# Optimization experiments

Hardware: AMD Instinct MI355X
Metric: run time of the kernel (lower is better)

Reference implementation:

```python
import jax, jax.numpy as jnp
import numpy as np

TOP_P = 0.9
B, D, H, O, E = 8192, 1024, 2048, 1024, 8


def setup_inputs() -> dict:
    key = jax.random.key(0)
    ks = jax.random.split(key, 6)
    def init(k, shape, fan_in):
        return (jax.random.normal(k, shape, jnp.float32) * (fan_in ** -0.5)).astype(jnp.float32)
    return {
        "x": jax.random.normal(ks[0], (B, D), jnp.float32),
        "gate_w": init(ks[1], (D, E), D),
        "gate_b": jnp.zeros((E,), jnp.float32),
        "w1": init(ks[2], (E, D, H), D),
        "b1": jnp.zeros((E, H), jnp.float32),
        "w2": init(ks[3], (E, H, O), H),
        "b2": jnp.zeros((E, O), jnp.float32),
    }


def reference(x, gate_w, gate_b, w1, b1, w2, b2):
    # gate + softmax
    logits = x @ gate_w + gate_b                      # [B,E]
    probs = jax.nn.softmax(logits, axis=-1)
    # all-expert MLP (batched over experts); torch GELU default is exact (erf)
    h = jax.nn.gelu(jnp.einsum('bd,edh->beh', x, w1) + b1[None], approximate=False)
    all_out = jnp.einsum('beh,eho->beo', h, w2) + b2[None]  # [B,E,O]
    # routing (entropy) loss
    routing_loss = (-jnp.sum(probs * jnp.log(probs + 1e-8), axis=-1)).mean()
    # diversity (gram logdet) loss
    mean_probs = probs.mean(axis=0)[:, None]          # [E,1]
    expert_mean = all_out.mean(axis=0)                # [E,O]
    norm = jnp.linalg.norm(expert_mean, axis=1, keepdims=True) + 1e-6
    V = mean_probs * (expert_mean / norm)             # [E,O]
    gram = V @ V.T + 1e-6 * jnp.eye(E, dtype=V.dtype)
    diversity_loss = -jnp.linalg.slogdet(gram)[1]
    # top-p mask over experts
    order = jnp.argsort(-probs, axis=-1)              # descending
    p_sorted = jnp.take_along_axis(probs, order, axis=-1)
    cum = jnp.cumsum(p_sorted, axis=-1)
    mask = cum <= TOP_P
    mask = mask.at[:, 0].set(True)
    inv = jnp.argsort(order, axis=-1)                 # inverse permutation
    mask_orig = jnp.take_along_axis(mask, inv, axis=-1)
    # normalized masked combine
    mp = probs * mask_orig.astype(probs.dtype)
    wts = mp / (mp.sum(axis=-1, keepdims=True) + 1e-8)
    output = jnp.einsum('be,beo->bo', wts, all_out)
    return output, routing_loss, diversity_loss
```

## Files before the change

### kernel.cpp

```cpp
#include <hip/hip_runtime.h>
#include <cstdint>
#include <cstddef>
#include <cmath>

#define B_ 8192
#define D_ 1024
#define H_ 2048
#define O_ 1024
#define E_ 8

typedef __bf16 bf16;
typedef __bf16 bf16x8 __attribute__((ext_vector_type(8)));
typedef __bf16 bf16x4v __attribute__((ext_vector_type(4)));
typedef float f32x4 __attribute__((ext_vector_type(4)));

typedef __attribute__((address_space(1))) void gvoid;
typedef __attribute__((address_space(3))) void lvoid;

__device__ __forceinline__ void gload16(const void* g, void* l) {
  __builtin_amdgcn_global_load_lds((gvoid*)g, (lvoid*)l, 16u, 0, 0);
}

__device__ __forceinline__ float fast_erff(float x) {
  float ax = __builtin_fabsf(x);
  float t = 1.f / (1.f + 0.3275911f * ax);
  float p = t * (0.254829592f +
            t * (-0.284496736f +
            t * (1.421413741f +
            t * (-1.453152027f +
            t * 1.061405429f))));
  float r = 1.f - p * __expf(-ax * ax);
  return __builtin_copysignf(r, x);
}
__device__ __forceinline__ float gelu_exact(float v) {
  return 0.5f * v * (1.f + fast_erff(v * 0.70710678118654752f));
}

__global__ __launch_bounds__(256) void convert_x_kernel(const float* __restrict__ x,
                                                        bf16* __restrict__ xb) {
  size_t i = (size_t)blockIdx.x * 256 + threadIdx.x;
  float4 v = ((const float4*)x)[i];
  bf16x4v o;
  o[0] = (bf16)v.x; o[1] = (bf16)v.y; o[2] = (bf16)v.z; o[3] = (bf16)v.w;
  ((bf16x4v*)xb)[i] = o;
}

__global__ __launch_bounds__(256) void transpose_w_kernel(const float* __restrict__ w,
                                                          bf16* __restrict__ wt,
                                                          int R, int C) {
  __shared__ float tile[32][33];
  int e = blockIdx.z;
  int c0 = blockIdx.x * 32, r0 = blockIdx.y * 32;
  int tx = threadIdx.x, ty = threadIdx.y;
  const float* we = w + (size_t)e * R * C;
  bf16* wte = wt + (size_t)e * R * C;
#pragma unroll
  for (int k = 0; k < 4; ++k) {
    int r = ty + 8 * k;
    tile[r][tx] = we[(size_t)(r0 + r) * C + c0 + tx];
  }
  __syncthreads();
#pragma unroll
  for (int k = 0; k < 4; ++k) {
    int c = ty + 8 * k;
    wte[(size_t)(c0 + c) * R + r0 + tx] = (bf16)tile[tx][c];
  }
}

__global__ __launch_bounds__(256) void gating_kernel(const float* __restrict__ x,
                                                     const float* __restrict__ gw,
                                                     const float* __restrict__ gb,
                                                     float* __restrict__ probs,
                                                     float* __restrict__ wts,
                                                     float* __restrict__ ent) {
  int w = threadIdx.x >> 6, l = threadIdx.x & 63;
  int b = blockIdx.x * 4 + w;
  const float* xr = x + (size_t)b * D_;
  float acc[E_];
#pragma unroll
  for (int e = 0; e < E_; ++e) acc[e] = 0.f;
  for (int j = 0; j < D_ / 64; ++j) {
    int d = j * 64 + l;
    float xv = xr[d];
    const float* g = gw + (size_t)d * E_;
#pragma unroll
    for (int e = 0; e < E_; ++e) acc[e] += xv * g[e];
  }
#pragma unroll
  for (int off = 32; off; off >>= 1)
#pragma unroll
    for (int e = 0; e < E_; ++e) acc[e] += __shfl_down(acc[e], off);

  if (l == 0) {
    float lg[E_], p[E_];
    float mx = -1e30f;
#pragma unroll
    for (int e = 0; e < E_; ++e) { lg[e] = acc[e] + gb[e]; mx = fmaxf(mx, lg[e]); }
    float s = 0.f;
#pragma unroll
    for (int e = 0; e < E_; ++e) { p[e] = expf(lg[e] - mx); s += p[e]; }
    float inv = 1.f / s;
    float en = 0.f;
#pragma unroll
    for (int e = 0; e < E_; ++e) { p[e] *= inv; en -= p[e] * logf(p[e] + 1e-8f); }
    ent[b] = en;
#pragma unroll
    for (int e = 0; e < E_; ++e) probs[(size_t)b * E_ + e] = p[e];
    int idx[E_]; float ps[E_];
#pragma unroll
    for (int e = 0; e < E_; ++e) { idx[e] = e; ps[e] = p[e]; }
    for (int i = 0; i < E_ - 1; ++i)
      for (int j = 0; j < E_ - 1 - i; ++j)
        if (ps[j] < ps[j + 1]) {
          float tp = ps[j]; ps[j] = ps[j + 1]; ps[j + 1] = tp;
          int ti = idx[j]; idx[j] = idx[j + 1]; idx[j + 1] = ti;
        }
    float cum = 0.f; float mp[E_];
#pragma unroll
    for (int e = 0; e < E_; ++e) mp[e] = 0.f;
    for (int i = 0; i < E_; ++i) {
      cum += ps[i];
      bool m = (cum <= 0.9f) || (i == 0);
      if (m) mp[idx[i]] = ps[i];
    }
    float ssum = 0.f;
#pragma unroll
    for (int e = 0; e < E_; ++e) ssum += mp[e];
    float invs = 1.f / (ssum + 1e-8f);
#pragma unroll
    for (int e = 0; e < E_; ++e) wts[(size_t)b * E_ + e] = mp[e] * invs;
  }
}

__device__ __forceinline__ void gemm_loop_rs(const bf16* __restrict__ A,
                                             const bf16* __restrict__ Bt,
                                             int K, int rowBase, int colBase,
                                             bf16* lA, bf16* lB, f32x4 acc[4][4]) {
  const int tid = threadIdx.x;
  const int w = tid >> 6, l = tid & 63;
  const int wm = w >> 1, wn = w & 1;
  const int fm = l & 15, fc = l >> 4;
  const int lr = l >> 3;
  const int lc = l & 7;
  const bf16* gA = A + (size_t)(rowBase + w * 32 + lr) * K + lc * 8;
  const bf16* gB = Bt + (size_t)(colBase + w * 32 + lr) * K + lc * 8;
  const int wp = lc ^ lr;
  bf16* dA = lA + (w * 32 + lr) * 64 + wp * 8;
  bf16* dB = lB + (w * 32 + lr) * 64 + wp * 8;

  bf16x8 ra[4], rb[4];
  const int nIter = K >> 6;
#pragma unroll
  for (int i = 0; i < 4; ++i) {
    ra[i] = *(const bf16x8*)(gA + (size_t)(i * 8) * K);
    rb[i] = *(const bf16x8*)(gB + (size_t)(i * 8) * K);
  }
  for (int it = 0; it < nIter; ++it) {
    __syncthreads();
#pragma unroll
    for (int i = 0; i < 4; ++i) {
      *(bf16x8*)(dA + i * 512) = ra[i];
      *(bf16x8*)(dB + i * 512) = rb[i];
    }
    if (it + 1 < nIter) {
      const int k0 = (it + 1) << 6;
#pragma unroll
      for (int i = 0; i < 4; ++i) {
        ra[i] = *(const bf16x8*)(gA + (size_t)(i * 8) * K + k0);
        rb[i] = *(const bf16x8*)(gB + (size_t)(i * 8) * K + k0);
      }
    }
    __syncthreads();
#pragma unroll
    for (int kh = 0; kh < 2; ++kh) {
      bf16x8 af[4], bb[4];
#pragma unroll
      for (int mt = 0; mt < 4; ++mt) {
        int r = wm * 64 + mt * 16 + fm;
        int pos = (kh * 4 + fc) ^ (r & 7);
        af[mt] = *(const bf16x8*)(lA + r * 64 + pos * 8);
      }
#pragma unroll
      for (int nt = 0; nt < 4; ++nt) {
        int r = wn * 64 + nt * 16 + fm;
        int pos = (kh * 4 + fc) ^ (r & 7);
        bb[nt] = *(const bf16x8*)(lB + r * 64 + pos * 8);
      }
#pragma unroll
      for (int mt = 0; mt < 4; ++mt)
#pragma unroll
        for (int nt = 0; nt < 4; ++nt)
          acc[mt][nt] = __builtin_amdgcn_mfma_f32_16x16x32_bf16(af[mt], bb[nt], acc[mt][nt], 0, 0, 0);
    }
  }
}

__device__ __forceinline__ void gemm_loop(const bf16* __restrict__ A,
                                          const bf16* __restrict__ Bt,
                                          int K, int rowBase, int colBase,
                                          bf16* lA, bf16* lB, f32x4 acc[4][4]) {
  const int tid = threadIdx.x;
  const int w = tid >> 6, l = tid & 63;
  const int wm = w >> 1, wn = w & 1;
  const int fm = l & 15, fc = l >> 4;
  const int lr = l >> 2, lc = l & 3;
  const int sr0 = (w * 2 + 0) * 16 + lr;
  const int sr1 = (w * 2 + 1) * 16 + lr;
  const int cg0 = lc ^ ((sr0 >> 1) & 3);
  const int cg1 = lc ^ ((sr1 >> 1) & 3);
  const bf16* gA0 = A + (size_t)(rowBase + sr0) * K + cg0 * 8;
  const bf16* gA1 = A + (size_t)(rowBase + sr1) * K + cg1 * 8;
  const bf16* gB0 = Bt + (size_t)(colBase + sr0) * K + cg0 * 8;
  const bf16* gB1 = Bt + (size_t)(colBase + sr1) * K + cg1 * 8;
  bf16* lA0 = lA + (w * 2 + 0) * 512;
  bf16* lA1 = lA + (w * 2 + 1) * 512;
  bf16* lB0 = lB + (w * 2 + 0) * 512;
  bf16* lB1 = lB + (w * 2 + 1) * 512;

  for (int k0 = 0; k0 < K; k0 += 32) {
    __syncthreads();
    gload16(gA0 + k0, lA0);
    gload16(gA1 + k0, lA1);
    gload16(gB0 + k0, lB0);
    gload16(gB1 + k0, lB1);
    __syncthreads();

    bf16x8 af[4], bb[4];
#pragma unroll
    for (int mt = 0; mt < 4; ++mt) {
      int r = wm * 64 + mt * 16 + fm;
      af[mt] = *(const bf16x8*)(lA + (size_t)(r * 4 + (fc ^ ((r >> 1) & 3))) * 8);
    }
#pragma unroll
    for (int nt = 0; nt < 4; ++nt) {
      int r = wn * 64 + nt * 16 + fm;
      bb[nt] = *(const bf16x8*)(lB + (size_t)(r * 4 + (fc ^ ((r >> 1) & 3))) * 8);
    }
#pragma unroll
    for (int mt = 0; mt < 4; ++mt)
#pragma unroll
      for (int nt = 0; nt < 4; ++nt)
        acc[mt][nt] = __builtin_amdgcn_mfma_f32_16x16x32_bf16(af[mt], bb[nt], acc[mt][nt], 0, 0, 0);
  }
}

__global__ __launch_bounds__(256) void gemm1_v5_kernel(const bf16* __restrict__ xb,
                                                       const bf16* __restrict__ w1t,
                                                       const float* __restrict__ b1,
                                                       const float* __restrict__ wts,
                                                       bf16* __restrict__ h_chunk,
                                                       float* __restrict__ hsum,
                                                       int rowOffset, int Bc) {
  __shared__ bf16 smem[17408];
  bf16* lA = smem;
  bf16* lB = smem + 8192;
  f32x4 acc[4][4];
#pragma unroll
  for (int mt = 0; mt < 4; ++mt)
#pragma unroll
    for (int nt = 0; nt < 4; ++nt) acc[mt][nt] = 0.f;

  const int flat = blockIdx.y * 128 + blockIdx.x;
  const int xcd = flat & 7, lin = flat >> 3;
  const int cb = xcd * 16 + (lin & 15);
  const int rb = lin >> 4;
  const int colBase = cb * 128;
  const int rowLocal = rb * 128;
  const int rowGlobal = rowOffset + rowLocal;
  const int e = colBase >> 11;

  gemm_loop_rs(xb, w1t, D_, rowGlobal, colBase, lA, lB, acc);

  const int tid = threadIdx.x;
  const int w = tid >> 6, l = tid & 63;
  const int wm = w >> 1, wn = w & 1;
  const int fm = l & 15, fc = l >> 4;
  bf16* he = h_chunk + (size_t)e * Bc * H_;
  const int hc0 = colBase & (H_ - 1);

  float wgt[4][4];
#pragma unroll
  for (int mt = 0; mt < 4; ++mt)
#pragma unroll
    for (int i = 0; i < 4; ++i) {
      int gr = rowGlobal + wm * 64 + mt * 16 + fc * 4 + i;
      wgt[mt][i] = wts[(size_t)gr * E_ + e];
    }

  __syncthreads();
#pragma unroll
  for (int nt = 0; nt < 4; ++nt) {
    int c = wn * 64 + nt * 16 + fm;
    float bias = b1[colBase + c];
    float csum = 0.f;
#pragma unroll
    for (int mt = 0; mt < 4; ++mt) {
      int rbse = wm * 64 + mt * 16 + fc * 4;
#pragma unroll
      for (int i = 0; i < 4; ++i) {
        float v = gelu_exact(acc[mt][nt][i] + bias);
        csum += v;
        smem[(size_t)(rbse + i) * 136 + c] = (bf16)(v * wgt[mt][i]);
      }
    }
    csum += __shfl_down(csum, 32);
    csum += __shfl_down(csum, 16);
    if (fc == 0) atomicAdd(&hsum[colBase + c], csum);
  }
  __syncthreads();

#pragma unroll
  for (int j = 0; j < 8; ++j) {
    int row = j * 16 + (tid >> 4);
    int cchunk = tid & 15;
    bf16x8 v = *(const bf16x8*)(smem + (size_t)row * 136 + cchunk * 8);
    *(bf16x8*)(he + (size_t)(rowLocal + row) * H_ + hc0 + cchunk * 8) = v;
  }
}

template <int SPLIT>
__global__ __launch_bounds__(256) void gemm2_v5_kernel(const bf16* __restrict__ h_chunk,
                                                       const bf16* __restrict__ w2t,
                                                       const float* __restrict__ b2,
                                                       const float* __restrict__ wts,
                                                       float* __restrict__ out_chunk,
                                                       int rowOffset, int Bc) {
  __shared__ bf16 smem[16384];
  bf16* lA = smem;
  bf16* lB = smem + 8192;
  f32x4 acc[4][4];
#pragma unroll
  for (int mt = 0; mt < 4; ++mt)
#pragma unroll
    for (int nt = 0; nt < 4; ++nt) acc[mt][nt] = 0.f;

  const int colBase = blockIdx.x * 128;
  const int rowLocal = blockIdx.y * 128;
  const int s = blockIdx.z;
  const int g = E_ / SPLIT, e0 = s * g;

  for (int e = e0; e < e0 + g; ++e)
    gemm_loop_rs(h_chunk + (size_t)e * Bc * H_, w2t + (size_t)e * O_ * H_, H_,
                 rowLocal, colBase, lA, lB, acc);

  const int w = threadIdx.x >> 6, l = threadIdx.x & 63;
  const int wm = w >> 1, wn = w & 1;
  const int fm = l & 15, fc = l >> 4;
#pragma unroll
  for (int nt = 0; nt < 4; ++nt) {
    int gc = colBase + wn * 64 + nt * 16 + fm;
    float b2v[E_];
    if (s == 0) {
#pragma unroll
      for (int e = 0; e < E_; ++e) b2v[e] = b2[(size_t)e * O_ + gc];
    }
#pragma unroll
    for (int mt = 0; mt < 4; ++mt) {
      int lrb = rowLocal + wm * 64 + mt * 16 + fc * 4;
#pragma unroll
      for (int i = 0; i < 4; ++i) {
        int lr2 = lrb + i;
        float v = acc[mt][nt][i];
        if (s == 0) {
          const float4* wr = (const float4*)(wts + (size_t)(rowOffset + lr2) * E_);
          float4 w0 = wr[0], w1v = wr[1];
          v += w0.x * b2v[0] + w0.y * b2v[1] + w0.z * b2v[2] + w0.w * b2v[3] +
               w1v.x * b2v[4] + w1v.y * b2v[5] + w1v.z * b2v[6] + w1v.w * b2v[7];
        }
        float* op = out_chunk + (size_t)lr2 * O_ + gc;
        if (SPLIT == 1) *op = v;
        else atomicAdd(op, v);
      }
    }
  }
}

__global__ __launch_bounds__(256) void esum_kernel(const float* __restrict__ hsum,
                                                   const float* __restrict__ w2,
                                                   float* __restrict__ esum2) {
  int e = blockIdx.y;
  int o = blockIdx.x * 256 + threadIdx.x;
  const float* w2e = w2 + (size_t)e * H_ * O_;
  const float* hs = hsum + (size_t)e * H_;
  float a0 = 0.f, a1 = 0.f;
  for (int h = 0; h < H_; h += 2) {
    a0 += hs[h] * w2e[(size_t)h * O_ + o];
    a1 += hs[h + 1] * w2e[(size_t)(h + 1) * O_ + o];
  }
  esum2[(size_t)e * O_ + o] = a0 + a1;
}

__global__ __launch_bounds__(256) void gemm1_gelu_kernel(const bf16* __restrict__ xb,
                                                         const bf16* __restrict__ w1te,
                                                         const float* __restrict__ b1e,
                                                         bf16* __restrict__ h) {
  __shared__ bf16 lA[128 * 32];
  __shared__ bf16 lB[128 * 32];
  f32x4 acc[4][4];
#pragma unroll
  for (int mt = 0; mt < 4; ++mt)
#pragma unroll
    for (int nt = 0; nt < 4; ++nt) acc[mt][nt] = 0.f;

  int rowBase = blockIdx.y * 128, colBase = blockIdx.x * 128;
  gemm_loop(xb, w1te, D_, rowBase, colBase, lA, lB, acc);

  const int w = threadIdx.x >> 6, l = threadIdx.x & 63;
  const int wm = w >> 1, wn = w & 1;
#pragma unroll
  for (int mt = 0; mt < 4; ++mt)
#pragma unroll
    for (int nt = 0; nt < 4; ++nt) {
      int gc = colBase + wn * 64 + nt * 16 + (l & 15);
      float bias = b1e[gc];
#pragma unroll
      for (int i = 0; i < 4; ++i) {
        int gr = rowBase + wm * 64 + mt * 16 + (l >> 4) * 4 + i;
        float v = gelu_exact(acc[mt][nt][i] + bias);
        h[(size_t)gr * H_ + gc] = (bf16)v;
      }
    }
}

__global__ __launch_bounds__(256) void gemm2_fused_kernel(const bf16* __restrict__ h,
                                                          const bf16* __restrict__ w2te,
                                                          const float* __restrict__ b2e,
                                                          const float* __restrict__ wts,
                                                          int e,
                                                          float* __restrict__ out,
                                                          float* __restrict__ esum) {
  __shared__ bf16 lA[128 * 32];
  __shared__ bf16 lB[128 * 32];
  f32x4 acc[4][4];
#pragma unroll
  for (int mt = 0; mt < 4; ++mt)
#pragma unroll
    for (int nt = 0; nt < 4; ++nt) acc[mt][nt] = 0.f;

  int rowBase = blockIdx.y * 128, colBase = blockIdx.x * 128;
  gemm_loop(h, w2te, H_, rowBase, colBase, lA, lB, acc);

  const int w = threadIdx.x >> 6, l = threadIdx.x & 63;
  const int wm = w >> 1, wn = w & 1;
#pragma unroll
  for (int nt = 0; nt < 4; ++nt) {
    int gc = colBase + wn * 64 + nt * 16 + (l & 15);
    float bias = b2e[gc];
    float csum = 0.f;
#pragma unroll
    for (int mt = 0; mt < 4; ++mt) {
      int grb = rowBase + wm * 64 + mt * 16 + (l >> 4) * 4;
#pragma unroll
      for (int i = 0; i < 4; ++i) {
        int gr = grb + i;
        float v = acc[mt][nt][i] + bias;
        csum += v;
        float wgt = wts[(size_t)gr * E_ + e];
        float* op = out + (size_t)gr * O_ + gc;
        *op += wgt * v;
      }
    }
    csum += __shfl_down(csum, 32);
    csum += __shfl_down(csum, 16);
    if ((l >> 4) == 0) atomicAdd(&esum[(size_t)e * O_ + gc], csum);
  }
}

template <int MODE>
__global__ __launch_bounds__(256) void scalars_kernel(const float* __restrict__ probs,
                                                      const float* __restrict__ ent,
                                                      const float* __restrict__ esum,
                                                      const float* __restrict__ b2,
                                                      float* __restrict__ outs) {
  __shared__ float red[256];
  __shared__ float Vsh[E_][O_ + 8];
  __shared__ float mp_sh[E_], norm_sh[E_];
  __shared__ float gram[E_][E_];
  int t = threadIdx.x;

  float s = 0.f;
  for (int i = t; i < B_; i += 256) s += ent[i];
  red[t] = s; __syncthreads();
  for (int off = 128; off; off >>= 1) { if (t < off) red[t] += red[t + off]; __syncthreads(); }
  if (t == 0) outs[0] = red[0] / (float)B_;
  __syncthreads();

  float mp[E_];
#pragma unroll
  for (int e = 0; e < E_; ++e) mp[e] = 0.f;
  for (int i = t; i < B_; i += 256) {
#pragma unroll
    for (int e = 0; e < E_; ++e) mp[e] += probs[(size_t)i * E_ + e];
  }
  for (int e = 0; e < E_; ++e) {
    red[t] = mp[e]; __syncthreads();
    for (int off = 128; off; off >>= 1) { if (t < off) red[t] += red[t + off]; __syncthreads(); }
    if (t == 0) mp_sh[e] = red[0] / (float)B_;
    __syncthreads();
  }

  for (int e = 0; e < E_; ++e) {
    float ss = 0.f;
    for (int o = t; o < O_; o += 256) {
      float m = esum[(size_t)e * O_ + o] / (float)B_;
      if (MODE == 1) m += b2[(size_t)e * O_ + o];
      ss += m * m;
    }
    red[t] = ss; __syncthreads();
    for (int off = 128; off; off >>= 1) { if (t < off) red[t] += red[t + off]; __syncthreads(); }
    if (t == 0) norm_sh[e] = sqrtf(red[0]) + 1e-6f;
    __syncthreads();
  }

  for (int e = 0; e < E_; ++e)
    for (int o = t; o < O_; o += 256) {
      float m = esum[(size_t)e * O_ + o] / (float)B_;
      if (MODE == 1) m += b2[(size_t)e * O_ + o];
      Vsh[e][o] = mp_sh[e] * m / norm_sh[e];
    }
  __syncthreads();

  if (t < 64) {
    int i = t >> 3, j = t & 7;
    float g = 0.f;
    for (int o = 0; o < O_; ++o) g += Vsh[i][o] * Vsh[j][o];
    if (i == j) g += 1e-6f;
    gram[i][j] = g;
  }
  __syncthreads();

  if (t == 0) {
    double a[E_][E_];
    for (int i = 0; i < E_; ++i) for (int j = 0; j < E_; ++j) a[i][j] = (double)gram[i][j];
    double ld = 0.0;
    for (int k = 0; k < E_; ++k) {
      int p = k; double mx = fabs(a[k][k]);
      for (int i = k + 1; i < E_; ++i) if (fabs(a[i][k]) > mx) { mx = fabs(a[i][k]); p = i; }
      if (p != k) for (int j = 0; j < E_; ++j) { double tmp = a[k][j]; a[k][j] = a[p][j]; a[p][j] = tmp; }
      ld += log(fabs(a[k][k]));
      double inv = 1.0 / a[k][k];
      for (int i = k + 1; i < E_; ++i) {
        double f = a[i][k] * inv;
        for (int j = k; j < E_; ++j) a[i][j] -= f * a[k][j];
      }
    }
    outs[1] = (float)(-ld);
  }
}

extern "C" void kernel_launch(void* const* d_in, const int* in_sizes, int n_in,
                              void* d_out, int out_size, void* d_ws, size_t ws_size,
                              hipStream_t stream) {
  const float* x  = (const float*)d_in[0];
  const float* gw = (const float*)d_in[1];
  const float* gb = (const float*)d_in[2];
  const float* w1 = (const float*)d_in[3];
  const float* b1 = (const float*)d_in[4];
  const float* w2 = (const float*)d_in[5];
  const float* b2 = (const float*)d_in[6];
  float* out = (float*)d_out;

  char* ws = (char*)d_ws;
  size_t need = 0;
  bf16* xb    = (bf16*)(ws + need); need += (size_t)B_ * D_ * 2;
  bf16* w1t   = (bf16*)(ws + need); need += (size_t)E_ * D_ * H_ * 2;
  bf16* w2t   = (bf16*)(ws + need); need += (size_t)E_ * H_ * O_ * 2;
  float* wts  = (float*)(ws + need); need += (size_t)B_ * E_ * 4;
  float* probs= (float*)(ws + need); need += (size_t)B_ * E_ * 4;
  float* ent  = (float*)(ws + need); need += (size_t)B_ * 4;
  float* hsum = (float*)(ws + need); need += (size_t)E_ * H_ * 4;
  float* esum = (float*)(ws + need); need += (size_t)E_ * O_ * 4;
  size_t need_common = need;
  bf16* h_chunk = (bf16*)(ws + need);

  int NC = 0;
  for (int nc = 1; nc <= 8; nc <<= 1) {
    size_t tot = need_common + (size_t)E_ * (B_ / nc) * H_ * 2;
    if (ws_size >= tot) { NC = nc; break; }
  }

  convert_x_kernel<<<(B_ * D_ / 4) / 256, 256, 0, stream>>>(x, xb);
  transpose_w_kernel<<<dim3(H_ / 32, D_ / 32, E_), dim3(32, 8), 0, stream>>>(w1, w1t, D_, H_);
  transpose_w_kernel<<<dim3(O_ / 32, H_ / 32, E_), dim3(32, 8), 0, stream>>>(w2, w2t, H_, O_);
  gating_kernel<<<B_ / 4, 256, 0, stream>>>(x, gw, gb, probs, wts, ent);

  if (NC > 0) {
    const int Bc = B_ / NC;
    const int SPLIT = (NC == 1) ? 2 : (NC == 2) ? 4 : 8;
    hipMemsetAsync(hsum, 0, (size_t)E_ * H_ * sizeof(float), stream);
    hipMemsetAsync(out, 0, (size_t)B_ * O_ * sizeof(float), stream);
    for (int c = 0; c < NC; ++c) {
      int rowOffset = c * Bc;
      gemm1_v5_kernel<<<dim3(128, Bc / 128), 256, 0, stream>>>(
          xb, w1t, b1, wts, h_chunk, hsum, rowOffset, Bc);
      float* out_chunk = out + (size_t)rowOffset * O_;
      dim3 g2(O_ / 128, Bc / 128, SPLIT);
      switch (SPLIT) {
        case 2: gemm2_v5_kernel<2><<<g2, 256, 0, stream>>>(h_chunk, w2t, b2, wts, out_chunk, rowOffset, Bc); break;
        case 4: gemm2_v5_kernel<4><<<g2, 256, 0, stream>>>(h_chunk, w2t, b2, wts, out_chunk, rowOffset, Bc); break;
        case 8: gemm2_v5_kernel<8><<<g2, 256, 0, stream>>>(h_chunk, w2t, b2, wts, out_chunk, rowOffset, Bc); break;
      }
    }
    esum_kernel<<<dim3(O_ / 256, E_), 256, 0, stream>>>(hsum, w2, esum);
    scalars_kernel<1><<<1, 256, 0, stream>>>(probs, ent, esum, b2, out + (size_t)B_ * O_);
  } else {
    bf16* he = (bf16*)(ws + need_common);
    if (ws_size < need_common + (size_t)B_ * H_ * 2) return;
    hipMemsetAsync(out, 0, (size_t)B_ * O_ * sizeof(float), stream);
    hipMemsetAsync(esum, 0, (size_t)E_ * O_ * sizeof(float), stream);
    for (int e = 0; e < E_; ++e) {
      gemm1_gelu_kernel<<<dim3(H_ / 128, B_ / 128), 256, 0, stream>>>(
          xb, w1t + (size_t)e * H_ * D_, b1 + (size_t)e * H_, he);
      gemm2_fused_kernel<<<dim3(O_ / 128, B_ / 128), 256, 0, stream>>>(
          he, w2t + (size_t)e * O_ * H_, b2 + (size_t)e * O_, wts, e, out, esum);
    }
    scalars_kernel<0><<<1, 256, 0, stream>>>(probs, ent, esum, b2, out + (size_t)B_ * O_);
  }
}
```

Baseline: 1.171 ms.

## Replace GEMM kernels with 256x256-tile, 8-wave, double-buffered direct-to-LDS pipelined versions

Both expert GEMMs move from 128x128 tiles with 4 waves and register-staged LDS loads to 256x256 tiles with 8 waves. The new kernels use global_load_lds async copies into double-buffered shared memory. They are split into half-K phases with explicit barriers, waitcnt and setprio around the MFMA blocks, so loads of the next tiles overlap compute. Block-to-tile mapping is remapped per XCD for cache locality. This raises arithmetic intensity and hides memory latency, at the cost of 128KB LDS per block (one block per CU) and more register pressure for the larger accumulator.

```diff
diff --git a/kernel.cpp b/kernel.cpp
--- a/kernel.cpp
+++ b/kernel.cpp
@@ -132,65 +132,299 @@
   }
 }
 
-__device__ __forceinline__ void gemm_loop_rs(const bf16* __restrict__ A,
-                                             const bf16* __restrict__ Bt,
-                                             int K, int rowBase, int colBase,
-                                             bf16* lA, bf16* lB, f32x4 acc[4][4]) {
+
+__device__ __forceinline__ void stage_half(const bf16* __restrict__ src, int ld,
+                                           int kOff, bf16* ldsHalf,
+                                           int w, int row16, int posG) {
+#pragma unroll
+  for (int c2 = 0; c2 < 2; ++c2) {
+    const int call = w * 2 + c2;
+    const int r = call * 16 + row16;
+    const int gchunk = posG ^ ((r >> 1) & 3);
+    gload16(src + (size_t)r * ld + kOff + gchunk * 8, ldsHalf + call * 512);
+  }
+}
+
+__device__ __forceinline__ void phase_pre_mfma() {
+  __builtin_amdgcn_s_barrier();
+  asm volatile("s_waitcnt lgkmcnt(0)" ::: "memory");
+  __builtin_amdgcn_sched_barrier(0);
+  __builtin_amdgcn_s_setprio(1);
+}
+__device__ __forceinline__ void phase_post_mfma() {
+  __builtin_amdgcn_s_setprio(0);
+  __builtin_amdgcn_s_barrier();
+}
+
+#define MFMA_QUAD(MB)                                                                   \
+  _Pragma("unroll") for (int m_ = 0; m_ < 4; ++m_)                                      \
+  _Pragma("unroll") for (int n_ = 0; n_ < 4; ++n_)                                      \
+    acc[(MB) + m_][n_] =                                                                \
+        __builtin_amdgcn_mfma_f32_16x16x32_bf16(afr[m_], bfr[n_], acc[(MB) + m_][n_], 0, 0, 0);
+
+__global__ __launch_bounds__(512) void gemm1_v6_kernel(const bf16* __restrict__ xb,
+                                                       const bf16* __restrict__ w1t,
+                                                       const float* __restrict__ b1,
+                                                       const float* __restrict__ wts,
+                                                       bf16* __restrict__ h_chunk,
+                                                       float* __restrict__ hsum,
+                                                       int rowOffset, int Bc, int nRow) {
+  __shared__ bf16 smem[65536];
   const int tid = threadIdx.x;
   const int w = tid >> 6, l = tid & 63;
-  const int wm = w >> 1, wn = w & 1;
+  const int wm = w >> 2, wn = w & 3;
   const int fm = l & 15, fc = l >> 4;
-  const int lr = l >> 3;
-  const int lc = l & 7;
-  const bf16* gA = A + (size_t)(rowBase + w * 32 + lr) * K + lc * 8;
-  const bf16* gB = Bt + (size_t)(colBase + w * 32 + lr) * K + lc * 8;
-  const int wp = lc ^ lr;
-  bf16* dA = lA + (w * 32 + lr) * 64 + wp * 8;
-  bf16* dB = lB + (w * 32 + lr) * 64 + wp * 8;
-
-  bf16x8 ra[4], rb[4];
-  const int nIter = K >> 6;
-#pragma unroll
-  for (int i = 0; i < 4; ++i) {
-    ra[i] = *(const bf16x8*)(gA + (size_t)(i * 8) * K);
-    rb[i] = *(const bf16x8*)(gB + (size_t)(i * 8) * K);
-  }
-  for (int it = 0; it < nIter; ++it) {
+  const int posOff = (fc ^ ((fm >> 1) & 3)) * 8;
+  const int row16 = l >> 2, posG = l & 3;
+
+  const int flat = blockIdx.x;
+  const int xcd = flat & 7, lin = flat >> 3;
+  const int cb = xcd * 8 + lin / nRow;
+  const int rb = lin % nRow;
+  const int colBase = cb * 256;
+  const int rowGlobal = rowOffset + rb * 256;
+  const int e = colBase >> 11;
+
+  f32x4 acc[8][4];
+#pragma unroll
+  for (int m = 0; m < 8; ++m)
+#pragma unroll
+    for (int n = 0; n < 4; ++n) acc[m][n] = 0.f;
+
+  const bf16* Ag = xb + (size_t)rowGlobal * D_;
+  const bf16* Bg = w1t + (size_t)colBase * D_;
+
+  stage_half(Ag, D_, 0,  smem,          w, row16, posG);
+  stage_half(Bg, D_, 0,  smem + 16384,  w, row16, posG);
+  stage_half(Ag, D_, 32, smem + 8192,   w, row16, posG);
+  stage_half(Bg, D_, 32, smem + 24576,  w, row16, posG);
+  stage_half(Ag, D_, 64, smem + 32768,  w, row16, posG);
+  stage_half(Bg, D_, 64, smem + 49152,  w, row16, posG);
+  asm volatile("s_waitcnt vmcnt(4)" ::: "memory");
+  __builtin_amdgcn_s_barrier();
+
+  const int nt = D_ / 64;
+  bf16x8 afr[4], bfr[4];
+#pragma unroll 2
+  for (int t = 0; t < nt; ++t) {
+    const int p = t & 1;
+    bf16* bufA = smem + p * 32768;
+    bf16* bufB = bufA + 16384;
+    bf16* nbufA = smem + (p ^ 1) * 32768;
+    bf16* nbufB = nbufA + 16384;
+    const bf16* laneA = bufA + (size_t)(wm * 128 + fm) * 32 + posOff;
+    const bf16* laneB = bufB + (size_t)(wn * 64 + fm) * 32 + posOff;
+
+#pragma unroll
+    for (int n = 0; n < 4; ++n) bfr[n] = *(const bf16x8*)(laneB + n * 512);
+#pragma unroll
+    for (int m = 0; m < 4; ++m) afr[m] = *(const bf16x8*)(laneA + m * 512);
+    if (t + 1 < nt) stage_half(Ag, D_, (t + 1) * 64 + 32, nbufA + 8192, w, row16, posG);
+    phase_pre_mfma();
+    MFMA_QUAD(0)
+    phase_post_mfma();
+
+#pragma unroll
+    for (int m = 0; m < 4; ++m) afr[m] = *(const bf16x8*)(laneA + 2048 + m * 512);
+    if (t + 1 < nt) stage_half(Bg, D_, (t + 1) * 64 + 32, nbufB + 8192, w, row16, posG);
+    phase_pre_mfma();
+    MFMA_QUAD(4)
+    phase_post_mfma();
+
+#pragma unroll
+    for (int n = 0; n < 4; ++n) bfr[n] = *(const bf16x8*)(laneB + 8192 + n * 512);
+#pragma unroll
+    for (int m = 0; m < 4; ++m) afr[m] = *(const bf16x8*)(laneA + 8192 + m * 512);
+    if (t + 2 < nt) stage_half(Ag, D_, (t + 2) * 64, bufA, w, row16, posG);
+    phase_pre_mfma();
+    MFMA_QUAD(0)
+    phase_post_mfma();
+
+#pragma unroll
+    for (int m = 0; m < 4; ++m) afr[m] = *(const bf16x8*)(laneA + 10240 + m * 512);
+    if (t + 2 < nt) stage_half(Bg, D_, (t + 2) * 64, bufB, w, row16, posG);
+    __builtin_amdgcn_s_barrier();
+    asm volatile("s_waitcnt lgkmcnt(0)" ::: "memory");
+    __builtin_amdgcn_sched_barrier(0);
+    __builtin_amdgcn_s_setprio(1);
+    MFMA_QUAD(4)
+    __builtin_amdgcn_s_setprio(0);
+    if (t < nt - 2) asm volatile("s_waitcnt vmcnt(4)" ::: "memory");
+    else            asm volatile("s_waitcnt vmcnt(0)" ::: "memory");
+    __builtin_amdgcn_s_barrier();
+  }
+
+  __syncthreads();
+  float wgt[8][4];
+#pragma unroll
+  for (int m = 0; m < 8; ++m)
+#pragma unroll
+    for (int i = 0; i < 4; ++i)
+      wgt[m][i] = wts[(size_t)(rowGlobal + wm * 128 + m * 16 + fc * 4 + i) * E_ + e];
+
+  bf16* he = h_chunk + (size_t)e * Bc * H_;
+  const int hc0 = colBase & (H_ - 1);
+  const int rowLocal = rb * 256;
+
+#pragma unroll
+  for (int hh = 0; hh < 2; ++hh) {
+    if (wm == hh) {
+#pragma unroll
+      for (int n = 0; n < 4; ++n) {
+        const int col = wn * 64 + n * 16 + fm;
+        const float bias = b1[colBase + col];
+        float csum = 0.f;
+#pragma unroll
+        for (int m = 0; m < 8; ++m) {
+          const int rbse = m * 16 + fc * 4;
+#pragma unroll
+          for (int i = 0; i < 4; ++i) {
+            float v = gelu_exact(acc[m][n][i] + bias);
+            csum += v;
+            smem[(size_t)(rbse + i) * 264 + col] = (bf16)(v * wgt[m][i]);
+          }
+        }
+        csum += __shfl_down(csum, 32);
+        csum += __shfl_down(csum, 16);
+        if (fc == 0) atomicAdd(&hsum[colBase + col], csum);
+      }
+    }
     __syncthreads();
 #pragma unroll
-    for (int i = 0; i < 4; ++i) {
-      *(bf16x8*)(dA + i * 512) = ra[i];
-      *(bf16x8*)(dB + i * 512) = rb[i];
-    }
-    if (it + 1 < nIter) {
-      const int k0 = (it + 1) << 6;
+    for (int j = 0; j < 8; ++j) {
+      const int u = j * 512 + tid;
+      const int row = u >> 5, ch = u & 31;
+      bf16x8 v = *(const bf16x8*)(smem + (size_t)row * 264 + ch * 8);
+      *(bf16x8*)(he + (size_t)(rowLocal + hh * 128 + row) * H_ + hc0 + ch * 8) = v;
+    }
+    __syncthreads();
+  }
+}
+
+template <int SPLIT>
+__global__ __launch_bounds__(512) void gemm2_v6_kernel(const bf16* __restrict__ h_chunk,
+                                                       const bf16* __restrict__ w2t,
+                                                       const float* __restrict__ b2,
+                                                       const float* __restrict__ wts,
+                                                       float* __restrict__ out_chunk,
+                                                       int rowOffset, int Bc, int nRow) {
+  __shared__ bf16 smem[65536];
+  const int tid = threadIdx.x;
+  const int w = tid >> 6, l = tid & 63;
+  const int wm = w >> 2, wn = w & 3;
+  const int fm = l & 15, fc = l >> 4;
+  const int posOff = (fc ^ ((fm >> 1) & 3)) * 8;
+  const int row16 = l >> 2, posG = l & 3;
+
+  const int flat = blockIdx.x;
+  const int xcd = flat & 7, lin = flat >> 3;
+  const int cb = xcd >> 1;
+  const int rb = (xcd & 1) * (nRow >> 1) + lin;
+  const int colBase = cb * 256;
+  const int rowLocal = rb * 256;
+  const int s = blockIdx.y;
+  constexpr int g = E_ / SPLIT;
+  const int e0 = s * g;
+  constexpr int nt = g * (H_ / 64);
+
+  f32x4 acc[8][4];
+#pragma unroll
+  for (int m = 0; m < 8; ++m)
+#pragma unroll
+    for (int n = 0; n < 4; ++n) acc[m][n] = 0.f;
+
+  const bf16* hA = h_chunk + (size_t)rowLocal * H_;
+  const bf16* wB = w2t + (size_t)colBase * H_;
+  const size_t strideA = (size_t)Bc * H_;
+  const size_t strideB = (size_t)O_ * H_;
+  auto srcA = [&](int tt) { return hA + (size_t)(e0 + (tt >> 5)) * strideA; };
+  auto srcB = [&](int tt) { return wB + (size_t)(e0 + (tt >> 5)) * strideB; };
+  auto koff = [&](int tt) { return (tt & 31) * 64; };
+
+  stage_half(srcA(0), H_, koff(0),      smem,          w, row16, posG);
+  stage_half(srcB(0), H_, koff(0),      smem + 16384,  w, row16, posG);
+  stage_half(srcA(0), H_, koff(0) + 32, smem + 8192,   w, row16, posG);
+  stage_half(srcB(0), H_, koff(0) + 32, smem + 24576,  w, row16, posG);
+  stage_half(srcA(1), H_, koff(1),      smem + 32768,  w, row16, posG);
+  stage_half(srcB(1), H_, koff(1),      smem + 49152,  w, row16, posG);
+  asm volatile("s_waitcnt vmcnt(4)" ::: "memory");
+  __builtin_amdgcn_s_barrier();
+
+  bf16x8 afr[4], bfr[4];
+#pragma unroll 2
+  for (int t = 0; t < nt; ++t) {
+    const int p = t & 1;
+    bf16* bufA = smem + p * 32768;
+    bf16* bufB = bufA + 16384;
+    bf16* nbufA = smem + (p ^ 1) * 32768;
+    bf16* nbufB = nbufA + 16384;
+    const bf16* laneA = bufA + (size_t)(wm * 128 + fm) * 32 + posOff;
+    const bf16* laneB = bufB + (size_t)(wn * 64 + fm) * 32 + posOff;
+
+#pragma unroll
+    for (int n = 0; n < 4; ++n) bfr[n] = *(const bf16x8*)(laneB + n * 512);
+#pragma unroll
+    for (int m = 0; m < 4; ++m) afr[m] = *(const bf16x8*)(laneA + m * 512);
+    if (t + 1 < nt) stage_half(srcA(t + 1), H_, koff(t + 1) + 32, nbufA + 8192, w, row16, posG);
+    phase_pre_mfma();
+    MFMA_QUAD(0)
+    phase_post_mfma();
+
+#pragma unroll
+    for (int m = 0; m < 4; ++m) afr[m] = *(const bf16x8*)(laneA + 2048 + m * 512);
+    if (t + 1 < nt) stage_half(srcB(t + 1), H_, koff(t + 1) + 32, nbufB + 8192, w, row16, posG);
+    phase_pre_mfma();
+    MFMA_QUAD(4)
+    phase_post_mfma();
+
+#pragma unroll
+    for (int n = 0; n < 4; ++n) bfr[n] = *(const bf16x8*)(laneB + 8192 + n * 512);
+#pragma unroll
+    for (int m = 0; m < 4; ++m) afr[m] = *(const bf16x8*)(laneA + 8192 + m * 512);
+    if (t + 2 < nt) stage_half(srcA(t + 2), H_, koff(t + 2), bufA, w, row16, posG);
+    phase_pre_mfma();
+    MFMA_QUAD(0)
+    phase_post_mfma();
+
+#pragma unroll
+    for (int m = 0; m < 4; ++m) afr[m] = *(const bf16x8*)(laneA + 10240 + m * 512);
+    if (t + 2 < nt) stage_half(srcB(t + 2), H_, koff(t + 2), bufB, w, row16, posG);
+    __builtin_amdgcn_s_barrier();
+    asm volatile("s_waitcnt lgkmcnt(0)" ::: "memory");
+    __builtin_amdgcn_sched_barrier(0);
+    __builtin_amdgcn_s_setprio(1);
+    MFMA_QUAD(4)
+    __builtin_amdgcn_s_setprio(0);
+    if (t < nt - 2) asm volatile("s_waitcnt vmcnt(4)" ::: "memory");
+    else            asm volatile("s_waitcnt vmcnt(0)" ::: "memory");
+    __builtin_amdgcn_s_barrier();
+  }
+
+#pragma unroll
+  for (int n = 0; n < 4; ++n) {
+    const int gc = colBase + wn * 64 + n * 16 + fm;
+    float b2v[E_];
+    if (s == 0) {
+#pragma unroll
+      for (int ee = 0; ee < E_; ++ee) b2v[ee] = b2[(size_t)ee * O_ + gc];
+    }
+#pragma unroll
+    for (int m = 0; m < 8; ++m) {
+      const int lrb = rowLocal + wm * 128 + m * 16 + fc * 4;
 #pragma unroll
       for (int i = 0; i < 4; ++i) {
-        ra[i] = *(const bf16x8*)(gA + (size_t)(i * 8) * K + k0);
-        rb[i] = *(const bf16x8*)(gB + (size_t)(i * 8) * K + k0);
+        const int lr2 = lrb + i;
+        float v = acc[m][n][i];
+        if (s == 0) {
+          const float4* wr = (const float4*)(wts + (size_t)(rowOffset + lr2) * E_);
+          float4 w0 = wr[0], w1v = wr[1];
+          v += w0.x * b2v[0] + w0.y * b2v[1] + w0.z * b2v[2] + w0.w * b2v[3] +
+               w1v.x * b2v[4] + w1v.y * b2v[5] + w1v.z * b2v[6] + w1v.w * b2v[7];
+        }
+        float* op = out_chunk + (size_t)lr2 * O_ + gc;
+        if (SPLIT == 1) *op = v;
+        else atomicAdd(op, v);
       }
-    }
-    __syncthreads();
-#pragma unroll
-    for (int kh = 0; kh < 2; ++kh) {
-      bf16x8 af[4], bb[4];
-#pragma unroll
-      for (int mt = 0; mt < 4; ++mt) {
-        int r = wm * 64 + mt * 16 + fm;
-        int pos = (kh * 4 + fc) ^ (r & 7);
-        af[mt] = *(const bf16x8*)(lA + r * 64 + pos * 8);
-      }
-#pragma unroll
-      for (int nt = 0; nt < 4; ++nt) {
-        int r = wn * 64 + nt * 16 + fm;
-        int pos = (kh * 4 + fc) ^ (r & 7);
-        bb[nt] = *(const bf16x8*)(lB + r * 64 + pos * 8);
-      }
-#pragma unroll
-      for (int mt = 0; mt < 4; ++mt)
-#pragma unroll
-        for (int nt = 0; nt < 4; ++nt)
-          acc[mt][nt] = __builtin_amdgcn_mfma_f32_16x16x32_bf16(af[mt], bb[nt], acc[mt][nt], 0, 0, 0);
     }
   }
 }
@@ -244,152 +478,6 @@
   }
 }
 
-__global__ __launch_bounds__(256) void gemm1_v5_kernel(const bf16* __restrict__ xb,
-                                                       const bf16* __restrict__ w1t,
-                                                       const float* __restrict__ b1,
-                                                       const float* __restrict__ wts,
-                                                       bf16* __restrict__ h_chunk,
-                                                       float* __restrict__ hsum,
-                                                       int rowOffset, int Bc) {
-  __shared__ bf16 smem[17408];
-  bf16* lA = smem;
-  bf16* lB = smem + 8192;
-  f32x4 acc[4][4];
-#pragma unroll
-  for (int mt = 0; mt < 4; ++mt)
-#pragma unroll
-    for (int nt = 0; nt < 4; ++nt) acc[mt][nt] = 0.f;
-
-  const int flat = blockIdx.y * 128 + blockIdx.x;
-  const int xcd = flat & 7, lin = flat >> 3;
-  const int cb = xcd * 16 + (lin & 15);
-  const int rb = lin >> 4;
-  const int colBase = cb * 128;
-  const int rowLocal = rb * 128;
-  const int rowGlobal = rowOffset + rowLocal;
-  const int e = colBase >> 11;
-
-  gemm_loop_rs(xb, w1t, D_, rowGlobal, colBase, lA, lB, acc);
-
-  const int tid = threadIdx.x;
-  const int w = tid >> 6, l = tid & 63;
-  const int wm = w >> 1, wn = w & 1;
-  const int fm = l & 15, fc = l >> 4;
-  bf16* he = h_chunk + (size_t)e * Bc * H_;
-  const int hc0 = colBase & (H_ - 1);
-
-  float wgt[4][4];
-#pragma unroll
-  for (int mt = 0; mt < 4; ++mt)
-#pragma unroll
-    for (int i = 0; i < 4; ++i) {
-      int gr = rowGlobal + wm * 64 + mt * 16 + fc * 4 + i;
-      wgt[mt][i] = wts[(size_t)gr * E_ + e];
-    }
-
-  __syncthreads();
-#pragma unroll
-  for (int nt = 0; nt < 4; ++nt) {
-    int c = wn * 64 + nt * 16 + fm;
-    float bias = b1[colBase + c];
-    float csum = 0.f;
-#pragma unroll
-    for (int mt = 0; mt < 4; ++mt) {
-      int rbse = wm * 64 + mt * 16 + fc * 4;
-#pragma unroll
-      for (int i = 0; i < 4; ++i) {
-        float v = gelu_exact(acc[mt][nt][i] + bias);
-        csum += v;
-        smem[(size_t)(rbse + i) * 136 + c] = (bf16)(v * wgt[mt][i]);
-      }
-    }
-    csum += __shfl_down(csum, 32);
-    csum += __shfl_down(csum, 16);
-    if (fc == 0) atomicAdd(&hsum[colBase + c], csum);
-  }
-  __syncthreads();
-
-#pragma unroll
-  for (int j = 0; j < 8; ++j) {
-    int row = j * 16 + (tid >> 4);
-    int cchunk = tid & 15;
-    bf16x8 v = *(const bf16x8*)(smem + (size_t)row * 136 + cchunk * 8);
-    *(bf16x8*)(he + (size_t)(rowLocal + row) * H_ + hc0 + cchunk * 8) = v;
-  }
-}
-
-template <int SPLIT>
-__global__ __launch_bounds__(256) void gemm2_v5_kernel(const bf16* __restrict__ h_chunk,
-                                                       const bf16* __restrict__ w2t,
-                                                       const float* __restrict__ b2,
-                                                       const float* __restrict__ wts,
-                                                       float* __restrict__ out_chunk,
-                                                       int rowOffset, int Bc) {
-  __shared__ bf16 smem[16384];
-  bf16* lA = smem;
-  bf16* lB = smem + 8192;
-  f32x4 acc[4][4];
-#pragma unroll
-  for (int mt = 0; mt < 4; ++mt)
-#pragma unroll
-    for (int nt = 0; nt < 4; ++nt) acc[mt][nt] = 0.f;
-
-  const int colBase = blockIdx.x * 128;
-  const int rowLocal = blockIdx.y * 128;
-  const int s = blockIdx.z;
-  const int g = E_ / SPLIT, e0 = s * g;
-
-  for (int e = e0; e < e0 + g; ++e)
-    gemm_loop_rs(h_chunk + (size_t)e * Bc * H_, w2t + (size_t)e * O_ * H_, H_,
-                 rowLocal, colBase, lA, lB, acc);
-
-  const int w = threadIdx.x >> 6, l = threadIdx.x & 63;
-  const int wm = w >> 1, wn = w & 1;
-  const int fm = l & 15, fc = l >> 4;
-#pragma unroll
-  for (int nt = 0; nt < 4; ++nt) {
-    int gc = colBase + wn * 64 + nt * 16 + fm;
-    float b2v[E_];
-    if (s == 0) {
-#pragma unroll
-      for (int e = 0; e < E_; ++e) b2v[e] = b2[(size_t)e * O_ + gc];
-    }
-#pragma unroll
-    for (int mt = 0; mt < 4; ++mt) {
-      int lrb = rowLocal + wm * 64 + mt * 16 + fc * 4;
-#pragma unroll
-      for (int i = 0; i < 4; ++i) {
-        int lr2 = lrb + i;
-        float v = acc[mt][nt][i];
-        if (s == 0) {
-          const float4* wr = (const float4*)(wts + (size_t)(rowOffset + lr2) * E_);
-          float4 w0 = wr[0], w1v = wr[1];
-          v += w0.x * b2v[0] + w0.y * b2v[1] + w0.z * b2v[2] + w0.w * b2v[3] +
-               w1v.x * b2v[4] + w1v.y * b2v[5] + w1v.z * b2v[6] + w1v.w * b2v[7];
-        }
-        float* op = out_chunk + (size_t)lr2 * O_ + gc;
-        if (SPLIT == 1) *op = v;
-        else atomicAdd(op, v);
-      }
-    }
-  }
-}
-
-__global__ __launch_bounds__(256) void esum_kernel(const float* __restrict__ hsum,
-                                                   const float* __restrict__ w2,
-                                                   float* __restrict__ esum2) {
-  int e = blockIdx.y;
-  int o = blockIdx.x * 256 + threadIdx.x;
-  const float* w2e = w2 + (size_t)e * H_ * O_;
-  const float* hs = hsum + (size_t)e * H_;
-  float a0 = 0.f, a1 = 0.f;
-  for (int h = 0; h < H_; h += 2) {
-    a0 += hs[h] * w2e[(size_t)h * O_ + o];
-    a1 += hs[h + 1] * w2e[(size_t)(h + 1) * O_ + o];
-  }
-  esum2[(size_t)e * O_ + o] = a0 + a1;
-}
-
 __global__ __launch_bounds__(256) void gemm1_gelu_kernel(const bf16* __restrict__ xb,
                                                          const bf16* __restrict__ w1te,
                                                          const float* __restrict__ b1e,
@@ -548,6 +636,21 @@
   }
 }
 
+__global__ __launch_bounds__(256) void esum_kernel(const float* __restrict__ hsum,
+                                                   const float* __restrict__ w2,
+                                                   float* __restrict__ esum2) {
+  int e = blockIdx.y;
+  int o = blockIdx.x * 256 + threadIdx.x;
+  const float* w2e = w2 + (size_t)e * H_ * O_;
+  const float* hs = hsum + (size_t)e * H_;
+  float a0 = 0.f, a1 = 0.f;
+  for (int h = 0; h < H_; h += 2) {
+    a0 += hs[h] * w2e[(size_t)h * O_ + o];
+    a1 += hs[h + 1] * w2e[(size_t)(h + 1) * O_ + o];
+  }
+  esum2[(size_t)e * O_ + o] = a0 + a1;
+}
+
 extern "C" void kernel_launch(void* const* d_in, const int* in_sizes, int n_in,
                               void* d_out, int out_size, void* d_ws, size_t ws_size,
                               hipStream_t stream) {
@@ -586,19 +689,20 @@
 
   if (NC > 0) {
     const int Bc = B_ / NC;
+    const int nRow = Bc / 256;
     const int SPLIT = (NC == 1) ? 2 : (NC == 2) ? 4 : 8;
     hipMemsetAsync(hsum, 0, (size_t)E_ * H_ * sizeof(float), stream);
     hipMemsetAsync(out, 0, (size_t)B_ * O_ * sizeof(float), stream);
     for (int c = 0; c < NC; ++c) {
       int rowOffset = c * Bc;
-      gemm1_v5_kernel<<<dim3(128, Bc / 128), 256, 0, stream>>>(
-          xb, w1t, b1, wts, h_chunk, hsum, rowOffset, Bc);
+      gemm1_v6_kernel<<<64 * nRow, 512, 0, stream>>>(
+          xb, w1t, b1, wts, h_chunk, hsum, rowOffset, Bc, nRow);
       float* out_chunk = out + (size_t)rowOffset * O_;
-      dim3 g2(O_ / 128, Bc / 128, SPLIT);
+      dim3 g2(4 * nRow, SPLIT);
       switch (SPLIT) {
-        case 2: gemm2_v5_kernel<2><<<g2, 256, 0, stream>>>(h_chunk, w2t, b2, wts, out_chunk, rowOffset, Bc); break;
-        case 4: gemm2_v5_kernel<4><<<g2, 256, 0, stream>>>(h_chunk, w2t, b2, wts, out_chunk, rowOffset, Bc); break;
-        case 8: gemm2_v5_kernel<8><<<g2, 256, 0, stream>>>(h_chunk, w2t, b2, wts, out_chunk, rowOffset, Bc); break;
+        case 2: gemm2_v6_kernel<2><<<g2, 512, 0, stream>>>(h_chunk, w2t, b2, wts, out_chunk, rowOffset, Bc, nRow); break;
+        case 4: gemm2_v6_kernel<4><<<g2, 512, 0, stream>>>(h_chunk, w2t, b2, wts, out_chunk, rowOffset, Bc, nRow); break;
+        case 8: gemm2_v6_kernel<8><<<g2, 512, 0, stream>>>(h_chunk, w2t, b2, wts, out_chunk, rowOffset, Bc, nRow); break;
       }
     }
     esum_kernel<<<dim3(O_ / 256, E_), 256, 0, stream>>>(hsum, w2, esum);
```

New measurement: 1.166 ms. No clear change (-0.4%).
